# Kernel tuning notes

Measured on AMD Instinct MI355X. Metric: run time of the kernel, lower is better.

Reference implementation:

```python
import jax, jax.numpy as jnp
import numpy as np

K = 3        # kernel_size
PAD = 1      # padding ('same' for stride 1)
RANK = 53    # CP rank from compression=10: round(27*32*64/(10*(9+32+64)))


def _kaiming_uniform(key, shape, fan_in):
    # matches nn.init.kaiming_uniform_(a=sqrt(5)): bound = 1/sqrt(fan_in)
    bound = 1.0 / np.sqrt(fan_in)
    return jax.random.uniform(key, shape, jnp.float32, -bound, bound)


def setup_inputs() -> dict:
    key = jax.random.key(0)
    ks = jax.random.split(key, 7)
    B, Cin, Cout, H, W, D = 1, 32, 64, 56, 56, 56
    x = jax.random.normal(ks[0], (B, Cin, H, W, D), jnp.float32)
    # CP factor matrices (fan_in = second dim for torch's 2D kaiming)
    U_kh = _kaiming_uniform(ks[1], (K, RANK), RANK)
    U_kw = _kaiming_uniform(ks[2], (K, RANK), RANK)
    U_kd = _kaiming_uniform(ks[3], (K, RANK), RANK)
    U_cin = _kaiming_uniform(ks[4], (Cin, RANK), RANK)
    U_cout = _kaiming_uniform(ks[5], (RANK, Cout), Cout)
    bias = jax.random.normal(ks[6], (Cout,), jnp.float32)
    return {"x": x, "U_kh": U_kh, "U_kw": U_kw, "U_kd": U_kd,
            "U_cin": U_cin, "U_cout": U_cout, "bias": bias}


def reference(x, U_kh, U_kw, U_kd, U_cin, U_cout, bias):
    B, C, H, W, D = x.shape
    xp = jnp.pad(x, ((0, 0), (0, 0), (PAD, PAD), (PAD, PAD), (PAD, PAD)))
    # im2col patches: patches[i,j,l,b,c,x,y,z] = xp[b,c,x+i,y+j,z+l]
    # (same values/ordering as torch unfold(2).unfold(3).unfold(4), stride=1)
    patches = jnp.stack([
        xp[:, :, i:i + H, j:j + W, l:l + D]
        for i in range(K) for j in range(K) for l in range(K)
    ]).reshape(K, K, K, B, C, H, W, D)
    # CP tensor-network contraction (legs: k_h,k_w,k_d,c_in share rank r -> c_out)
    out = jnp.einsum('ijlbcxyz,ir,jr,lr,cr,ro->boxyz',
                     patches, U_kh, U_kw, U_kd, U_cin, U_cout,
                     optimize=True)
    return out + bias[None, :, None, None, None]
```

## Files before the change

kernel.cpp:

```cpp
#include <hip/hip_runtime.h>


#define NP 175616
#define NP2 87808
#define NP4 43904
#define HSTR 3136
#define H2 1568
#define H4 784
#define W2 28
#define W4 14
#define QH 784
#define CIN 32
#define RK 53
#define COUT 64
#define SCR 53

__global__ __launch_bounds__(256) void k0_t(const float* __restrict__ Ucin,
                                            float* __restrict__ Ut)
{
    int t = blockIdx.x * 256 + threadIdx.x;
    if (t < RK * CIN) {
        int r = t >> 5, c = t & 31;
        Ut[t] = Ucin[c * RK + r];
    }
}

__global__ __launch_bounds__(256) void k1d(
    const float* __restrict__ x, const float* __restrict__ Ut,
    const float* __restrict__ Ukd, float* __restrict__ T1d)
{
    const int lane = threadIdx.x & 63;
    const int row  = blockIdx.x * 4 + (threadIdx.x >> 6);
    const int p    = row * 56 + lane;
    const bool act = (lane < 56);

    float xv[CIN];
#pragma unroll
    for (int c = 0; c < CIN; ++c) xv[c] = act ? x[c * NP + p] : 0.f;

#pragma unroll 2
    for (int r = 0; r < RK; ++r) {
        const float* U = Ut + r * CIN;
        float acc = 0.f;
#pragma unroll
        for (int c = 0; c < CIN; ++c) acc += xv[c] * U[c];
        float lm = __shfl_up(acc, 1, 64);
        float rp = __shfl_down(acc, 1, 64);
        if (lane == 0)  lm = 0.f;
        if (lane == 55) rp = 0.f;
        float res = lm * Ukd[r] + acc * Ukd[RK + r] + rp * Ukd[2 * RK + r];
        if (act) T1d[(size_t)r * NP + p] = res;
    }
}

__global__ __launch_bounds__(512, 4) void k3wh4(
    const float4* __restrict__ Ta, const float* __restrict__ Ucout,
    const float* __restrict__ bias, const float* __restrict__ Ukh,
    const float* __restrict__ Ukw, float4* __restrict__ Out)
{
    __shared__ float4 tld[RK][64];

    const int lane = threadIdx.x & 63;
    const int wv   = threadIdx.x >> 6;

    const int nwg = gridDim.x;
    const int qx = nwg >> 3, rx = nwg & 7;
    const int xcd = blockIdx.x & 7, loc = blockIdx.x >> 3;
    const int swz = ((xcd < rx) ? xcd * (qx + 1) : rx * (qx + 1) + (xcd - rx) * qx) + loc;

    const int q4 = swz * 64 + lane;
    const int h  = q4 / H4;
    const int rm = q4 - h * H4;
    const int w  = rm / W4;
    const bool hm = (h > 0), hp = (h < 55);
    const bool wm = (w > 0), wp = (w < 55);
    const int om = hm ? -H4 : 0;
    const int op = hp ?  H4 : 0;
    const int oa = wm ? -W4 : 0;
    const int oc = wp ?  W4 : 0;

    const float4* Sq = Ta + q4;

#pragma unroll 2
    for (int r = wv; r < RK; r += 8) {
        const float4* S = Sq + (size_t)r * NP4;
        const float kw0 = wm ? Ukw[r] : 0.f;
        const float kw1 = Ukw[RK + r];
        const float kw2 = wp ? Ukw[2 * RK + r] : 0.f;
        const float kh0 = hm ? Ukh[r] : 0.f;
        const float kh1 = Ukh[RK + r];
        const float kh2 = hp ? Ukh[2 * RK + r] : 0.f;

        float4 v00 = S[om + oa], v01 = S[om], v02 = S[om + oc];
        float4 v10 = S[oa],      v11 = S[0],  v12 = S[oc];
        float4 v20 = S[op + oa], v21 = S[op], v22 = S[op + oc];

        float4 t;
        t.x = (v00.x * kw0 + v01.x * kw1 + v02.x * kw2) * kh0
            + (v10.x * kw0 + v11.x * kw1 + v12.x * kw2) * kh1
            + (v20.x * kw0 + v21.x * kw1 + v22.x * kw2) * kh2;
        t.y = (v00.y * kw0 + v01.y * kw1 + v02.y * kw2) * kh0
            + (v10.y * kw0 + v11.y * kw1 + v12.y * kw2) * kh1
            + (v20.y * kw0 + v21.y * kw1 + v22.y * kw2) * kh2;
        t.z = (v00.z * kw0 + v01.z * kw1 + v02.z * kw2) * kh0
            + (v10.z * kw0 + v11.z * kw1 + v12.z * kw2) * kh1
            + (v20.z * kw0 + v21.z * kw1 + v22.z * kw2) * kh2;
        t.w = (v00.w * kw0 + v01.w * kw1 + v02.w * kw2) * kh0
            + (v10.w * kw0 + v11.w * kw1 + v12.w * kw2) * kh1
            + (v20.w * kw0 + v21.w * kw1 + v22.w * kw2) * kh2;
        tld[r][lane] = t;
    }
    __syncthreads();

    const int og = wv << 3;
    float4 a[8];
#pragma unroll
    for (int o = 0; o < 8; ++o) {
        float b = bias[og + o];
        a[o].x = b; a[o].y = b; a[o].z = b; a[o].w = b;
    }
#pragma unroll 2
    for (int r = 0; r < RK; ++r) {
        float4 t = tld[r][lane];
        const float* Ur = Ucout + r * COUT + og;
#pragma unroll
        for (int o = 0; o < 8; ++o) {
            float u = Ur[o];
            a[o].x += t.x * u; a[o].y += t.y * u;
            a[o].z += t.z * u; a[o].w += t.w * u;
        }
    }
#pragma unroll
    for (int o = 0; o < 8; ++o)
        Out[(size_t)(og + o) * NP4 + q4] = a[o];
}


__global__ __launch_bounds__(256) void k1_chunk(
    const float* __restrict__ x, const float* __restrict__ Ucin,
    float* T, int r0, int nr)
{
    __shared__ float sU[11 * CIN];
    const int tid = threadIdx.x;
    for (int t = tid; t < nr * CIN; t += 256) {
        int lr = t >> 5, c = t & 31;
        sU[t] = Ucin[c * RK + (r0 + lr)];
    }
    __syncthreads();
    const int p = blockIdx.x * 256 + tid;
    float xv[CIN];
#pragma unroll
    for (int c = 0; c < CIN; ++c) xv[c] = x[c * NP + p];
#pragma unroll 1
    for (int lr = 0; lr < nr; ++lr) {
        float acc = 0.f;
#pragma unroll
        for (int c = 0; c < CIN; ++c) acc += xv[c] * sU[lr * CIN + c];
        T[(size_t)(SCR + lr) * NP + p] = acc;
    }
}

__global__ __launch_bounds__(256) void k2_chunk(
    const float* __restrict__ Ukh, const float* __restrict__ Ukw,
    const float* __restrict__ Ukd, float* T, int r0)
{
    __shared__ float sIn[5800];
    __shared__ float sA[5600];
    const int lr = blockIdx.z;
    const int r  = r0 + lr;
    const int h0 = blockIdx.x * 8, w0 = blockIdx.y * 8;
    const int tid = threadIdx.x;
    const float kh0 = Ukh[r], kh1 = Ukh[RK + r], kh2 = Ukh[2 * RK + r];
    const float kw0 = Ukw[r], kw1 = Ukw[RK + r], kw2 = Ukw[2 * RK + r];
    const float kd0 = Ukd[r], kd1 = Ukd[RK + r], kd2 = Ukd[2 * RK + r];
    const float* T1r = T + (size_t)(SCR + lr) * NP;

    for (int idx = tid; idx < 5800; idx += 256) {
        int d = idx % 58; int t2 = idx / 58; int ww = t2 % 10; int hh = t2 / 10;
        int gh = h0 + hh - 1, gw = w0 + ww - 1, gd = d - 1;
        float v = 0.f;
        if ((unsigned)gh < 56u && (unsigned)gw < 56u && (unsigned)gd < 56u)
            v = T1r[gh * HSTR + gw * 56 + gd];
        sIn[idx] = v;
    }
    __syncthreads();
    for (int idx = tid; idx < 5600; idx += 256) {
        int d = idx % 56; int t2 = idx / 56; int ww = t2 % 10; int hh = t2 / 10;
        const float* b = &sIn[(hh * 10 + ww) * 58 + d];
        sA[idx] = b[0] * kd0 + b[1] * kd1 + b[2] * kd2;
    }
    __syncthreads();
    const float k00 = kh0 * kw0, k01 = kh0 * kw1, k02 = kh0 * kw2;
    const float k10 = kh1 * kw0, k11 = kh1 * kw1, k12 = kh1 * kw2;
    const float k20 = kh2 * kw0, k21 = kh2 * kw1, k22 = kh2 * kw2;
    for (int idx = tid; idx < 3584; idx += 256) {
        int d = idx % 56; int t2 = idx / 56; int ww = t2 % 8; int hh = t2 / 8;
        const float* a = &sA[(hh * 10 + ww) * 56 + d];
        float acc = a[0]    * k00 + a[56]   * k01 + a[112]  * k02
                  + a[560]  * k10 + a[616]  * k11 + a[672]  * k12
                  + a[1120] * k20 + a[1176] * k21 + a[1232] * k22;
        T[(size_t)r * NP + (h0 + hh) * HSTR + (w0 + ww) * 56 + d] = acc;
    }
}

__global__ __launch_bounds__(256) void k3_out(
    float* T, const float* __restrict__ Ucout, const float* __restrict__ bias)
{
    __shared__ float sUo[RK * COUT];
    __shared__ float sB[COUT];
    const int tid = threadIdx.x;
    for (int t = tid; t < RK * COUT; t += 256) sUo[t] = Ucout[t];
    if (tid < COUT) sB[tid] = bias[tid];
    __syncthreads();
    const int p = blockIdx.x * 256 + tid;
    float acc[COUT];
#pragma unroll
    for (int o = 0; o < COUT; ++o) acc[o] = sB[o];
#pragma unroll 1
    for (int r = 0; r < RK; ++r) {
        float t = T[(size_t)r * NP + p];
        const float* Ur = &sUo[r * COUT];
#pragma unroll
        for (int o = 0; o < COUT; ++o) acc[o] += t * Ur[o];
    }
#pragma unroll
    for (int o = 0; o < COUT; ++o) T[(size_t)o * NP + p] = acc[o];
}


extern "C" void kernel_launch(void* const* d_in, const int* in_sizes, int n_in,
                              void* d_out, int out_size, void* d_ws, size_t ws_size,
                              hipStream_t stream)
{
    const float* x     = (const float*)d_in[0];
    const float* Ukh   = (const float*)d_in[1];
    const float* Ukw   = (const float*)d_in[2];
    const float* Ukd   = (const float*)d_in[3];
    const float* Ucin  = (const float*)d_in[4];
    const float* Ucout = (const float*)d_in[5];
    const float* bias  = (const float*)d_in[6];

    const size_t t1_bytes = (size_t)RK * NP * sizeof(float);

    if (ws_size >= t1_bytes + 8192) {
        float* T1 = (float*)d_ws;
        float* Ut = (float*)((char*)d_ws + t1_bytes);
        k0_t<<<7, 256, 0, stream>>>(Ucin, Ut);
        k1d<<<HSTR / 4, 256, 0, stream>>>(x, Ut, Ukd, T1);
        k3wh4<<<NP4 / 64, 512, 0, stream>>>((const float4*)T1, Ucout, bias, Ukh,
                                            Ukw, (float4*)d_out);
    } else {
        float* T = (float*)d_out;
        for (int r0 = 0; r0 < RK; r0 += 11) {
            int nr = (RK - r0 < 11) ? (RK - r0) : 11;
            k1_chunk<<<NP / 256, 256, 0, stream>>>(x, Ucin, T, r0, nr);
            k2_chunk<<<dim3(7, 7, nr), 256, 0, stream>>>(Ukh, Ukw, Ukd, T, r0);
        }
        k3_out<<<NP / 256, 256, 0, stream>>>(T, Ucout, bias);
    }
}
```

Baseline: 159.3 us.

## Pipeline W/H stencil loads with Cout contraction via double-buffered LDS

The final kernel used to compute all 53 rank slices of the W/H stencil into a full LDS tile, sync once, then run the rank-to-Cout matmul. It now processes ranks in groups of 8 with a two-slot LDS buffer. The global loads for the next group are issued before the current group's matmul, so memory latency can overlap with FMA work, and LDS use drops from 53 rows to 16. In exchange it adds six extra block barriers and holds nine float4 registers live across the matmul, which raises register pressure.

```diff
diff --git a/kernel.cpp b/kernel.cpp
--- a/kernel.cpp
+++ b/kernel.cpp
@@ -2,14 +2,10 @@
 
 
 #define NP 175616
-#define NP2 87808
 #define NP4 43904
 #define HSTR 3136
-#define H2 1568
 #define H4 784
-#define W2 28
 #define W4 14
-#define QH 784
 #define CIN 32
 #define RK 53
 #define COUT 64
@@ -53,12 +49,12 @@
     }
 }
 
-__global__ __launch_bounds__(512, 4) void k3wh4(
+__global__ __launch_bounds__(512, 4) void k3p(
     const float4* __restrict__ Ta, const float* __restrict__ Ucout,
     const float* __restrict__ bias, const float* __restrict__ Ukh,
     const float* __restrict__ Ukw, float4* __restrict__ Out)
 {
-    __shared__ float4 tld[RK][64];
+    __shared__ float4 tld[2][8][64];
 
     const int lane = threadIdx.x & 63;
     const int wv   = threadIdx.x >> 6;
@@ -81,58 +77,86 @@
 
     const float4* Sq = Ta + q4;
 
-#pragma unroll 2
-    for (int r = wv; r < RK; r += 8) {
-        const float4* S = Sq + (size_t)r * NP4;
-        const float kw0 = wm ? Ukw[r] : 0.f;
-        const float kw1 = Ukw[RK + r];
-        const float kw2 = wp ? Ukw[2 * RK + r] : 0.f;
-        const float kh0 = hm ? Ukh[r] : 0.f;
-        const float kh1 = Ukh[RK + r];
-        const float kh2 = hp ? Ukh[2 * RK + r] : 0.f;
-
-        float4 v00 = S[om + oa], v01 = S[om], v02 = S[om + oc];
-        float4 v10 = S[oa],      v11 = S[0],  v12 = S[oc];
-        float4 v20 = S[op + oa], v21 = S[op], v22 = S[op + oc];
-
-        float4 t;
-        t.x = (v00.x * kw0 + v01.x * kw1 + v02.x * kw2) * kh0
-            + (v10.x * kw0 + v11.x * kw1 + v12.x * kw2) * kh1
-            + (v20.x * kw0 + v21.x * kw1 + v22.x * kw2) * kh2;
-        t.y = (v00.y * kw0 + v01.y * kw1 + v02.y * kw2) * kh0
-            + (v10.y * kw0 + v11.y * kw1 + v12.y * kw2) * kh1
-            + (v20.y * kw0 + v21.y * kw1 + v22.y * kw2) * kh2;
-        t.z = (v00.z * kw0 + v01.z * kw1 + v02.z * kw2) * kh0
-            + (v10.z * kw0 + v11.z * kw1 + v12.z * kw2) * kh1
-            + (v20.z * kw0 + v21.z * kw1 + v22.z * kw2) * kh2;
-        t.w = (v00.w * kw0 + v01.w * kw1 + v02.w * kw2) * kh0
-            + (v10.w * kw0 + v11.w * kw1 + v12.w * kw2) * kh1
-            + (v20.w * kw0 + v21.w * kw1 + v22.w * kw2) * kh2;
-        tld[r][lane] = t;
-    }
-    __syncthreads();
-
-    const int og = wv << 3;
+    const int og = __builtin_amdgcn_readfirstlane((threadIdx.x >> 6) << 3);
+
     float4 a[8];
 #pragma unroll
     for (int o = 0; o < 8; ++o) {
         float b = bias[og + o];
         a[o].x = b; a[o].y = b; a[o].z = b; a[o].w = b;
     }
-#pragma unroll 2
-    for (int r = 0; r < RK; ++r) {
-        float4 t = tld[r][lane];
-        const float* Ur = Ucout + r * COUT + og;
-#pragma unroll
-        for (int o = 0; o < 8; ++o) {
-            float u = Ur[o];
-            a[o].x += t.x * u; a[o].y += t.y * u;
-            a[o].z += t.z * u; a[o].w += t.w * u;
-        }
-    }
+
+#define LOAD9(S) \
+    v00 = (S)[om + oa]; v01 = (S)[om]; v02 = (S)[om + oc]; \
+    v10 = (S)[oa];      v11 = (S)[0];  v12 = (S)[oc];      \
+    v20 = (S)[op + oa]; v21 = (S)[op]; v22 = (S)[op + oc];
+
+#define WHBLEND(t, r) { \
+    const float kw0 = wm ? Ukw[r] : 0.f; \
+    const float kw1 = Ukw[RK + (r)]; \
+    const float kw2 = wp ? Ukw[2 * RK + (r)] : 0.f; \
+    const float kh0 = hm ? Ukh[r] : 0.f; \
+    const float kh1 = Ukh[RK + (r)]; \
+    const float kh2 = hp ? Ukh[2 * RK + (r)] : 0.f; \
+    t.x = (v00.x * kw0 + v01.x * kw1 + v02.x * kw2) * kh0 \
+        + (v10.x * kw0 + v11.x * kw1 + v12.x * kw2) * kh1 \
+        + (v20.x * kw0 + v21.x * kw1 + v22.x * kw2) * kh2; \
+    t.y = (v00.y * kw0 + v01.y * kw1 + v02.y * kw2) * kh0 \
+        + (v10.y * kw0 + v11.y * kw1 + v12.y * kw2) * kh1 \
+        + (v20.y * kw0 + v21.y * kw1 + v22.y * kw2) * kh2; \
+    t.z = (v00.z * kw0 + v01.z * kw1 + v02.z * kw2) * kh0 \
+        + (v10.z * kw0 + v11.z * kw1 + v12.z * kw2) * kh1 \
+        + (v20.z * kw0 + v21.z * kw1 + v22.z * kw2) * kh2; \
+    t.w = (v00.w * kw0 + v01.w * kw1 + v02.w * kw2) * kh0 \
+        + (v10.w * kw0 + v11.w * kw1 + v12.w * kw2) * kh1 \
+        + (v20.w * kw0 + v21.w * kw1 + v22.w * kw2) * kh2; }
+
+    float4 v00, v01, v02, v10, v11, v12, v20, v21, v22;
+
+    {
+        const float4* S = Sq + (size_t)wv * NP4;
+        LOAD9(S);
+        float4 t;
+        WHBLEND(t, wv);
+        tld[0][wv][lane] = t;
+    }
+    __syncthreads();
+
+#pragma unroll
+    for (int g = 0; g < 7; ++g) {
+        const int rn = (g + 1) * 8 + wv;
+        const bool hn = (g < 6) && (rn < RK);
+        if (hn) {
+            const float4* S = Sq + (size_t)rn * NP4;
+            LOAD9(S);
+        }
+        const int n = (g == 6) ? 5 : 8;
+#pragma unroll
+        for (int rr = 0; rr < 8; ++rr) {
+            if (rr < n) {
+                float4 t = tld[g & 1][rr][lane];
+                const float* Ur = Ucout + (g * 8 + rr) * COUT + og;
+#pragma unroll
+                for (int o = 0; o < 8; ++o) {
+                    float u = Ur[o];
+                    a[o].x += t.x * u; a[o].y += t.y * u;
+                    a[o].z += t.z * u; a[o].w += t.w * u;
+                }
+            }
+        }
+        if (hn) {
+            float4 t;
+            WHBLEND(t, rn);
+            tld[(g + 1) & 1][wv][lane] = t;
+        }
+        if (g < 6) __syncthreads();
+    }
+
 #pragma unroll
     for (int o = 0; o < 8; ++o)
         Out[(size_t)(og + o) * NP4 + q4] = a[o];
+#undef LOAD9
+#undef WHBLEND
 }
 
 
@@ -247,8 +271,8 @@
         float* Ut = (float*)((char*)d_ws + t1_bytes);
         k0_t<<<7, 256, 0, stream>>>(Ucin, Ut);
         k1d<<<HSTR / 4, 256, 0, stream>>>(x, Ut, Ukd, T1);
-        k3wh4<<<NP4 / 64, 512, 0, stream>>>((const float4*)T1, Ucout, bias, Ukh,
-                                            Ukw, (float4*)d_out);
+        k3p<<<NP4 / 64, 512, 0, stream>>>((const float4*)T1, Ucout, bias, Ukh,
+                                          Ukw, (float4*)d_out);
     } else {
         float* T = (float*)d_out;
         for (int r0 = 0; r0 < RK; r0 += 11) {
```

Measured after the change: 208.1 us. 1.31x slower.
